# Optimization experiments

Measured on AMD Instinct MI355X. Metric: run time of the kernel, lower is better.

## Reference

```python
import jax, jax.numpy as jnp
import numpy as np
import math

BLOCK = 32
TAU = 0.1
INIT_SPARSITY = 0.1


def setup_inputs() -> dict:
    key = jax.random.key(0)
    k1, k2, k3, k4 = jax.random.split(key, 4)
    B, S, D_IN, D_OUT = 4, 2048, 4096, 4096
    x = jax.random.normal(k1, (B, S, D_IN), dtype=jnp.float32)
    # nn.Linear default init: uniform(-1/sqrt(in), 1/sqrt(in))
    bound = 1.0 / math.sqrt(D_IN)
    weight = jax.random.uniform(k2, (D_OUT, D_IN), minval=-bound, maxval=bound, dtype=jnp.float32)
    bias = jax.random.uniform(k3, (D_OUT,), minval=-bound, maxval=bound, dtype=jnp.float32)
    # scores init per _init_scores: randn*0.1 + logit(init_sparsity)
    target_logit = math.log(INIT_SPARSITY / (1.0 - INIT_SPARSITY))
    scores = jax.random.normal(k4, (D_OUT // BLOCK, D_IN // BLOCK), dtype=jnp.float32) * 0.1 + target_logit
    return {"x": x, "weight": weight, "bias": bias, "scores": scores}


def reference(x, weight, bias, scores):
    # block mask: sigmoid(scores) > tau, expanded 32x32 per block
    block_mask = (jax.nn.sigmoid(scores) > TAU).astype(weight.dtype)  # [O/32, I/32]
    full_mask = jnp.repeat(jnp.repeat(block_mask, BLOCK, axis=0), BLOCK, axis=1)  # [O, I]
    pruned_weight = weight * full_mask
    # F.linear: x @ W^T + b
    return jnp.einsum('bsi,oi->bso', x, pruned_weight) + bias
```

## Files before the change

kernel.cpp:

```cpp
#include <hip/hip_runtime.h>


#define BM 128
#define BN 128
#define BK 64

typedef __attribute__((ext_vector_type(8))) short bf16x8;
typedef __attribute__((ext_vector_type(4))) float f32x4;

__device__ __forceinline__ unsigned short f2bf(float f) {
    union { float f; unsigned u; } v; v.f = f;
    return (unsigned short)((v.u + 0x7FFFu + ((v.u >> 16) & 1u)) >> 16);
}

#define THRESH (-2.1972245773362196f)

__global__ __launch_bounds__(256)
void prep(const float* __restrict__ X, const float* __restrict__ W,
          const float* __restrict__ scores,
          unsigned short* __restrict__ Xb, unsigned short* __restrict__ Wb,
          unsigned long long* __restrict__ mbits,
          int M, int N, int K) {
    const int b   = blockIdx.x;
    const int tid = threadIdx.x;
    const int KBlk = K >> 5;

    if (b < M) {
        const float* src = X + (long)b * K;
        unsigned short* dst = Xb + (long)b * K;
        for (int k = tid * 4; k < K; k += 1024) {
            const float4 a = *(const float4*)(src + k);
            ushort4 p;
            p.x = f2bf(a.x); p.y = f2bf(a.y); p.z = f2bf(a.z); p.w = f2bf(a.w);
            *(ushort4*)(dst + k) = p;
        }
    } else if (b < M + N) {
        const int n = b - M;
        const float* src = W + (long)n * K;
        unsigned short* dst = Wb + (long)n * K;
        const float* srow = scores + (long)(n >> 5) * KBlk;
        for (int k = tid * 4; k < K; k += 1024) {
            if (srow[k >> 5] > THRESH) {
                const float4 a = *(const float4*)(src + k);
                ushort4 p;
                p.x = f2bf(a.x); p.y = f2bf(a.y); p.z = f2bf(a.z); p.w = f2bf(a.w);
                *(ushort4*)(dst + k) = p;
            }
        }
    } else {
        const int nb = (b - (M + N)) * 4 + (tid >> 6);
        const int l  = tid & 63;
        const unsigned long long b0 = __ballot(scores[(long)nb * KBlk + l] > THRESH);
        const unsigned long long b1 = __ballot(scores[(long)nb * KBlk + 64 + l] > THRESH);
        if (l == 0) { mbits[nb * 2] = b0; mbits[nb * 2 + 1] = b1; }
    }
}


__device__ __forceinline__ unsigned long long rfl64(unsigned long long v) {
    unsigned lo = __builtin_amdgcn_readfirstlane((unsigned)v);
    unsigned hi = __builtin_amdgcn_readfirstlane((unsigned)(v >> 32));
    return ((unsigned long long)hi << 32) | lo;
}

#define GLL16(g, l) __builtin_amdgcn_global_load_lds( \
    (const __attribute__((address_space(1))) void*)(g), \
    (__attribute__((address_space(3))) void*)(l), 16, 0, 0)

__global__ __launch_bounds__(256)
void mpl_main(const unsigned short* __restrict__ Xb,
              const unsigned short* __restrict__ Wb,
              const float* __restrict__ bias,
              const unsigned long long* __restrict__ mb,
              float* __restrict__ out, int M, int N, int K)
{
    __shared__ unsigned short sA[BM * BK];
    __shared__ unsigned short sB[BN * BK];

    const int tid  = threadIdx.x;
    const int lane = tid & 63;
    const int wave = tid >> 6;
    const int m0   = blockIdx.y * BM;
    const int n0   = blockIdx.x * BN;
    const int wm   = (wave & 1) * 64;
    const int wn   = (wave >> 1) * 64;
    const long K2  = (long)K * 2;

    const int nbb = n0 >> 5;
    unsigned long long mlo[4], mhi[4];
#pragma unroll
    for (int i = 0; i < 4; i++) {
        mlo[i] = rfl64(mb[(nbb + i) * 2]);
        mhi[i] = rfl64(mb[(nbb + i) * 2 + 1]);
    }

    f32x4 acc[4][4];
#pragma unroll
    for (int i = 0; i < 4; i++)
#pragma unroll
        for (int j = 0; j < 4; j++)
            acc[i][j] = (f32x4){0.f, 0.f, 0.f, 0.f};

    const int r8   = tid >> 3;
    const int cswz = ((tid & 7) ^ ((tid >> 3) & 7)) * 16;
    const char* gA = (const char*)Xb + (long)(m0 + r8) * K2 + cswz;
    const char* gB = (const char*)Wb + (long)(n0 + r8) * K2 + cswz;
    char* sAc = (char*)sA;
    char* sBc = (char*)sB;
    const int ldso = wave * 1024;

    const int fr   = lane & 15;
    const int cxor = lane & 7;
    const int kqc  = lane >> 4;
    const int rowA = wm + fr;
    const int rowB = wn + fr;

    int kb2 = 0;
    for (int half = 0; half < 2; ++half) {
        const unsigned long long w0 = half ? mhi[0] : mlo[0];
        const unsigned long long w1 = half ? mhi[1] : mlo[1];
        const unsigned long long w2 = half ? mhi[2] : mlo[2];
        const unsigned long long w3 = half ? mhi[3] : mlo[3];
        for (int q = 0; q < 32; ++q, ++kb2) {
            const unsigned p0 = (unsigned)(w0 >> (2 * q)) & 3;
            const unsigned p1 = (unsigned)(w1 >> (2 * q)) & 3;
            const unsigned p2 = (unsigned)(w2 >> (2 * q)) & 3;
            const unsigned p3 = (unsigned)(w3 >> (2 * q)) & 3;
            if (!(p0 | p1 | p2 | p3)) continue;

            const long ko = (long)kb2 * 128;
#pragma unroll
            for (int i = 0; i < 4; i++)
                GLL16(gA + (long)i * 32 * K2 + ko, sAc + i * 4096 + ldso);
            if (p0) GLL16(gB + 0L * 32 * K2 + ko, sBc + 0 * 4096 + ldso);
            if (p1) GLL16(gB + 1L * 32 * K2 + ko, sBc + 1 * 4096 + ldso);
            if (p2) GLL16(gB + 2L * 32 * K2 + ko, sBc + 2 * 4096 + ldso);
            if (p3) GLL16(gB + 3L * 32 * K2 + ko, sBc + 3 * 4096 + ldso);
            __syncthreads();

            const unsigned plo = (wave >> 1) ? p2 : p0;
            const unsigned phi = (wave >> 1) ? p3 : p1;

#pragma unroll
            for (int kbl = 0; kbl < 2; ++kbl) {
                if (!(((plo | phi) >> kbl) & 1)) continue;
                const int boff = ((kqc | (kbl << 2)) ^ cxor) * 16;

                bf16x8 af[4];
#pragma unroll
                for (int mi = 0; mi < 4; mi++)
                    af[mi] = *(const bf16x8*)(sAc + (rowA + mi * 16) * 128 + boff);

                if ((plo >> kbl) & 1) {
                    const bf16x8 bf0 = *(const bf16x8*)(sBc + (rowB + 0)  * 128 + boff);
                    const bf16x8 bf1 = *(const bf16x8*)(sBc + (rowB + 16) * 128 + boff);
#pragma unroll
                    for (int mi = 0; mi < 4; mi++) {
                        acc[mi][0] = __builtin_amdgcn_mfma_f32_16x16x32_bf16(af[mi], bf0, acc[mi][0], 0, 0, 0);
                        acc[mi][1] = __builtin_amdgcn_mfma_f32_16x16x32_bf16(af[mi], bf1, acc[mi][1], 0, 0, 0);
                    }
                }
                if ((phi >> kbl) & 1) {
                    const bf16x8 bf2 = *(const bf16x8*)(sBc + (rowB + 32) * 128 + boff);
                    const bf16x8 bf3 = *(const bf16x8*)(sBc + (rowB + 48) * 128 + boff);
#pragma unroll
                    for (int mi = 0; mi < 4; mi++) {
                        acc[mi][2] = __builtin_amdgcn_mfma_f32_16x16x32_bf16(af[mi], bf2, acc[mi][2], 0, 0, 0);
                        acc[mi][3] = __builtin_amdgcn_mfma_f32_16x16x32_bf16(af[mi], bf3, acc[mi][3], 0, 0, 0);
                    }
                }
            }
            __syncthreads();
        }
    }

    const int cn = lane & 15;
    const int rq = (lane >> 4) * 4;
#pragma unroll
    for (int ni = 0; ni < 4; ni++) {
        const int n = n0 + wn + ni * 16 + cn;
        const float b = bias[n];
#pragma unroll
        for (int mi = 0; mi < 4; mi++) {
#pragma unroll
            for (int r = 0; r < 4; r++) {
                const int m = m0 + wm + mi * 16 + rq + r;
                out[(long)m * N + n] = acc[mi][ni][r] + b;
            }
        }
    }
}


#define FBK 32
#define LDSS (FBK + 8)
__global__ __launch_bounds__(256, 2)
void mpl_gemm_fb(const float* __restrict__ X, const float* __restrict__ W,
                 const float* __restrict__ bias, const float* __restrict__ scores,
                 float* __restrict__ out, int M, int N, int K)
{
    __shared__ unsigned short sA[BM * LDSS];
    __shared__ unsigned short sB[BN * LDSS];
    const int tid = threadIdx.x;
    const int m0 = blockIdx.y * BM, n0 = blockIdx.x * BN;
    const int wave = tid >> 6, lane = tid & 63;
    const int wm = (wave & 1) * 64, wn = (wave >> 1) * 64;
    const int kblocks = K >> 5;
    f32x4 acc[4][4];
#pragma unroll
    for (int i = 0; i < 4; i++)
#pragma unroll
        for (int j = 0; j < 4; j++) acc[i][j] = (f32x4){0.f,0.f,0.f,0.f};
    int srow[4], sc4[4], snb[4];
#pragma unroll
    for (int i = 0; i < 4; i++) {
        int f = tid + 256 * i;
        srow[i] = f >> 3; sc4[i] = f & 7; snb[i] = (n0 + srow[i]) >> 5;
    }
    for (int k0 = 0; k0 < K; k0 += FBK) {
        const int kb = k0 >> 5;
#pragma unroll
        for (int i = 0; i < 4; i++) {
            const float4 v = *(const float4*)(X + (long)(m0 + srow[i]) * K + k0 + sc4[i] * 4);
            ushort4 p; p.x = f2bf(v.x); p.y = f2bf(v.y); p.z = f2bf(v.z); p.w = f2bf(v.w);
            *(ushort4*)&sA[srow[i] * LDSS + sc4[i] * 4] = p;
        }
#pragma unroll
        for (int i = 0; i < 4; i++) {
            const float msk = (scores[snb[i] * kblocks + kb] > THRESH) ? 1.0f : 0.0f;
            const float4 v = *(const float4*)(W + (long)(n0 + srow[i]) * K + k0 + sc4[i] * 4);
            ushort4 p; p.x = f2bf(v.x*msk); p.y = f2bf(v.y*msk); p.z = f2bf(v.z*msk); p.w = f2bf(v.w*msk);
            *(ushort4*)&sB[srow[i] * LDSS + sc4[i] * 4] = p;
        }
        __syncthreads();
        const int fr = lane & 15, kq = (lane >> 4) * 8;
        bf16x8 af[4], bfr[4];
#pragma unroll
        for (int mi = 0; mi < 4; mi++) af[mi] = *(const bf16x8*)&sA[(wm + mi*16 + fr) * LDSS + kq];
#pragma unroll
        for (int ni = 0; ni < 4; ni++) bfr[ni] = *(const bf16x8*)&sB[(wn + ni*16 + fr) * LDSS + kq];
#pragma unroll
        for (int mi = 0; mi < 4; mi++)
#pragma unroll
            for (int ni = 0; ni < 4; ni++)
                acc[mi][ni] = __builtin_amdgcn_mfma_f32_16x16x32_bf16(af[mi], bfr[ni], acc[mi][ni], 0,0,0);
        __syncthreads();
    }
    const int cn = lane & 15, rq = (lane >> 4) * 4;
#pragma unroll
    for (int ni = 0; ni < 4; ni++) {
        const int n = n0 + wn + ni * 16 + cn;
        const float b = bias[n];
#pragma unroll
        for (int mi = 0; mi < 4; mi++)
#pragma unroll
            for (int r = 0; r < 4; r++)
                out[(long)(m0 + wm + mi*16 + rq + r) * N + n] = acc[mi][ni][r] + b;
    }
}

extern "C" void kernel_launch(void* const* d_in, const int* in_sizes, int n_in,
                              void* d_out, int out_size, void* d_ws, size_t ws_size,
                              hipStream_t stream) {
    const float* X      = (const float*)d_in[0];
    const float* W      = (const float*)d_in[1];
    const float* bias   = (const float*)d_in[2];
    const float* scores = (const float*)d_in[3];
    float* out          = (float*)d_out;

    const int N = in_sizes[2];
    const int K = in_sizes[1] / N;
    const int M = in_sizes[0] / K;
    const int KB = K >> 5;
    const int NB = N >> 5;

    const size_t mk2 = (size_t)M * K * 2;
    const size_t nk2 = (size_t)N * K * 2;
    const size_t need = mk2 + nk2 + (size_t)NB * 16;

    if (ws_size >= need && KB == 128 && (M % 128) == 0 && (N % 128) == 0 &&
        (K % 1024) == 0 && (NB % 4) == 0) {
        unsigned short* Xb = (unsigned short*)d_ws;
        unsigned short* Wb = (unsigned short*)((char*)d_ws + mk2);
        unsigned long long* mbits = (unsigned long long*)((char*)d_ws + mk2 + nk2);

        prep<<<M + N + NB / 4, 256, 0, stream>>>(X, W, scores, Xb, Wb, mbits, M, N, K);

        dim3 grid(N / BN, M / BM);
        mpl_main<<<grid, dim3(256), 0, stream>>>(Xb, Wb, bias, mbits, out, M, N, K);
    } else {
        dim3 grid(N / BN, M / BM);
        mpl_gemm_fb<<<grid, dim3(256), 0, stream>>>(X, W, bias, scores, out, M, N, K);
    }
}
```

Baseline: 478.1 us.

## Double-buffer LDS tiles with prefetch, remap workgroups across XCDs, stride prep rows

```diff
diff --git a/kernel.cpp b/kernel.cpp
--- a/kernel.cpp
+++ b/kernel.cpp
@@ -25,30 +25,33 @@
     const int tid = threadIdx.x;
     const int KBlk = K >> 5;
 
-    if (b < M) {
-        const float* src = X + (long)b * K;
-        unsigned short* dst = Xb + (long)b * K;
-        for (int k = tid * 4; k < K; k += 1024) {
-            const float4 a = *(const float4*)(src + k);
-            ushort4 p;
-            p.x = f2bf(a.x); p.y = f2bf(a.y); p.z = f2bf(a.z); p.w = f2bf(a.w);
-            *(ushort4*)(dst + k) = p;
-        }
-    } else if (b < M + N) {
-        const int n = b - M;
-        const float* src = W + (long)n * K;
-        unsigned short* dst = Wb + (long)n * K;
-        const float* srow = scores + (long)(n >> 5) * KBlk;
-        for (int k = tid * 4; k < K; k += 1024) {
-            if (srow[k >> 5] > THRESH) {
+    if (b < 2048) {
+        for (int row = b; row < M; row += 2048) {
+            const float* src = X + (long)row * K;
+            unsigned short* dst = Xb + (long)row * K;
+            for (int k = tid * 4; k < K; k += 1024) {
                 const float4 a = *(const float4*)(src + k);
                 ushort4 p;
                 p.x = f2bf(a.x); p.y = f2bf(a.y); p.z = f2bf(a.z); p.w = f2bf(a.w);
                 *(ushort4*)(dst + k) = p;
             }
         }
+    } else if (b < 3072) {
+        for (int row = b - 2048; row < N; row += 1024) {
+            const float* src = W + (long)row * K;
+            unsigned short* dst = Wb + (long)row * K;
+            const float* srow = scores + (long)(row >> 5) * KBlk;
+            for (int k = tid * 4; k < K; k += 1024) {
+                if (srow[k >> 5] > THRESH) {
+                    const float4 a = *(const float4*)(src + k);
+                    ushort4 p;
+                    p.x = f2bf(a.x); p.y = f2bf(a.y); p.z = f2bf(a.z); p.w = f2bf(a.w);
+                    *(ushort4*)(dst + k) = p;
+                }
+            }
+        }
     } else {
-        const int nb = (b - (M + N)) * 4 + (tid >> 6);
+        const int nb = (b - 3072) * 4 + (tid >> 6);
         const int l  = tid & 63;
         const unsigned long long b0 = __ballot(scores[(long)nb * KBlk + l] > THRESH);
         const unsigned long long b1 = __ballot(scores[(long)nb * KBlk + 64 + l] > THRESH);
@@ -66,6 +69,17 @@
 #define GLL16(g, l) __builtin_amdgcn_global_load_lds( \
     (const __attribute__((address_space(1))) void*)(g), \
     (__attribute__((address_space(3))) void*)(l), 16, 0, 0)
+
+#define STAGE(sAbuf, sBbuf, ko) do { \
+    GLL16(gA + 0L * 32 * K2 + (ko), (sAbuf) + 0 * 4096 + ldso); \
+    GLL16(gA + 1L * 32 * K2 + (ko), (sAbuf) + 1 * 4096 + ldso); \
+    GLL16(gA + 2L * 32 * K2 + (ko), (sAbuf) + 2 * 4096 + ldso); \
+    GLL16(gA + 3L * 32 * K2 + (ko), (sAbuf) + 3 * 4096 + ldso); \
+    GLL16(gB + 0L * 32 * K2 + (ko), (sBbuf) + 0 * 4096 + ldso); \
+    GLL16(gB + 1L * 32 * K2 + (ko), (sBbuf) + 1 * 4096 + ldso); \
+    GLL16(gB + 2L * 32 * K2 + (ko), (sBbuf) + 2 * 4096 + ldso); \
+    GLL16(gB + 3L * 32 * K2 + (ko), (sBbuf) + 3 * 4096 + ldso); \
+} while (0)
 
 __global__ __launch_bounds__(256)
 void mpl_main(const unsigned short* __restrict__ Xb,
@@ -74,14 +88,24 @@
               const unsigned long long* __restrict__ mb,
               float* __restrict__ out, int M, int N, int K)
 {
-    __shared__ unsigned short sA[BM * BK];
-    __shared__ unsigned short sB[BN * BK];
+    __shared__ unsigned short sA0[BM * BK];
+    __shared__ unsigned short sB0[BN * BK];
+    __shared__ unsigned short sA1[BM * BK];
+    __shared__ unsigned short sB1[BN * BK];
 
     const int tid  = threadIdx.x;
     const int lane = tid & 63;
     const int wave = tid >> 6;
-    const int m0   = blockIdx.y * BM;
-    const int n0   = blockIdx.x * BN;
+
+    const int nwg = gridDim.x;
+    int L = blockIdx.x;
+    if ((nwg & 7) == 0) L = (L & 7) * (nwg >> 3) + (L >> 3);
+    const int nbx = N / BN;
+    const int bx = L % nbx;
+    const int by = L / nbx;
+
+    const int m0   = by * BM;
+    const int n0   = bx * BN;
     const int wm   = (wave & 1) * 64;
     const int wn   = (wave >> 1) * 64;
     const long K2  = (long)K * 2;
@@ -105,8 +129,10 @@
     const int cswz = ((tid & 7) ^ ((tid >> 3) & 7)) * 16;
     const char* gA = (const char*)Xb + (long)(m0 + r8) * K2 + cswz;
     const char* gB = (const char*)Wb + (long)(n0 + r8) * K2 + cswz;
-    char* sAc = (char*)sA;
-    char* sBc = (char*)sB;
+    char* sA0c = (char*)sA0;
+    char* sB0c = (char*)sB0;
+    char* sA1c = (char*)sA1;
+    char* sB1c = (char*)sB1;
     const int ldso = wave * 1024;
 
     const int fr   = lane & 15;
@@ -115,32 +141,33 @@
     const int rowA = wm + fr;
     const int rowB = wn + fr;
 
-    int kb2 = 0;
-    for (int half = 0; half < 2; ++half) {
-        const unsigned long long w0 = half ? mhi[0] : mlo[0];
-        const unsigned long long w1 = half ? mhi[1] : mlo[1];
-        const unsigned long long w2 = half ? mhi[2] : mlo[2];
-        const unsigned long long w3 = half ? mhi[3] : mlo[3];
-        for (int q = 0; q < 32; ++q, ++kb2) {
-            const unsigned p0 = (unsigned)(w0 >> (2 * q)) & 3;
-            const unsigned p1 = (unsigned)(w1 >> (2 * q)) & 3;
-            const unsigned p2 = (unsigned)(w2 >> (2 * q)) & 3;
-            const unsigned p3 = (unsigned)(w3 >> (2 * q)) & 3;
-            if (!(p0 | p1 | p2 | p3)) continue;
-
-            const long ko = (long)kb2 * 128;
-#pragma unroll
-            for (int i = 0; i < 4; i++)
-                GLL16(gA + (long)i * 32 * K2 + ko, sAc + i * 4096 + ldso);
-            if (p0) GLL16(gB + 0L * 32 * K2 + ko, sBc + 0 * 4096 + ldso);
-            if (p1) GLL16(gB + 1L * 32 * K2 + ko, sBc + 1 * 4096 + ldso);
-            if (p2) GLL16(gB + 2L * 32 * K2 + ko, sBc + 2 * 4096 + ldso);
-            if (p3) GLL16(gB + 3L * 32 * K2 + ko, sBc + 3 * 4096 + ldso);
-            __syncthreads();
-
-            const unsigned plo = (wave >> 1) ? p2 : p0;
-            const unsigned phi = (wave >> 1) ? p3 : p1;
-
+    STAGE(sA0c, sB0c, 0L);
+
+#pragma unroll 2
+    for (int s = 0; s < 64; ++s) {
+        if (s < 63) {
+            const long konext = (long)(s + 1) * 128;
+            if (s & 1) STAGE(sA0c, sB0c, konext);
+            else       STAGE(sA1c, sB1c, konext);
+            asm volatile("s_waitcnt vmcnt(8)" ::: "memory");
+        } else {
+            asm volatile("s_waitcnt vmcnt(0)" ::: "memory");
+        }
+        __builtin_amdgcn_s_barrier();
+        __builtin_amdgcn_sched_barrier(0);
+
+        const char* cA = (s & 1) ? sA1c : sA0c;
+        const char* cB = (s & 1) ? sB1c : sB0c;
+
+        const int hq = s & 31;
+        const unsigned p0 = (unsigned)(((s & 32) ? mhi[0] : mlo[0]) >> (2 * hq)) & 3;
+        const unsigned p1 = (unsigned)(((s & 32) ? mhi[1] : mlo[1]) >> (2 * hq)) & 3;
+        const unsigned p2 = (unsigned)(((s & 32) ? mhi[2] : mlo[2]) >> (2 * hq)) & 3;
+        const unsigned p3 = (unsigned)(((s & 32) ? mhi[3] : mlo[3]) >> (2 * hq)) & 3;
+        const unsigned plo = (wave >> 1) ? p2 : p0;
+        const unsigned phi = (wave >> 1) ? p3 : p1;
+
+        if (plo | phi) {
 #pragma unroll
             for (int kbl = 0; kbl < 2; ++kbl) {
                 if (!(((plo | phi) >> kbl) & 1)) continue;
@@ -149,11 +176,11 @@
                 bf16x8 af[4];
 #pragma unroll
                 for (int mi = 0; mi < 4; mi++)
-                    af[mi] = *(const bf16x8*)(sAc + (rowA + mi * 16) * 128 + boff);
+                    af[mi] = *(const bf16x8*)(cA + (rowA + mi * 16) * 128 + boff);
 
                 if ((plo >> kbl) & 1) {
-                    const bf16x8 bf0 = *(const bf16x8*)(sBc + (rowB + 0)  * 128 + boff);
-                    const bf16x8 bf1 = *(const bf16x8*)(sBc + (rowB + 16) * 128 + boff);
+                    const bf16x8 bf0 = *(const bf16x8*)(cB + (rowB + 0)  * 128 + boff);
+                    const bf16x8 bf1 = *(const bf16x8*)(cB + (rowB + 16) * 128 + boff);
 #pragma unroll
                     for (int mi = 0; mi < 4; mi++) {
                         acc[mi][0] = __builtin_amdgcn_mfma_f32_16x16x32_bf16(af[mi], bf0, acc[mi][0], 0, 0, 0);
@@ -161,8 +188,8 @@
                     }
                 }
                 if ((phi >> kbl) & 1) {
-                    const bf16x8 bf2 = *(const bf16x8*)(sBc + (rowB + 32) * 128 + boff);
-                    const bf16x8 bf3 = *(const bf16x8*)(sBc + (rowB + 48) * 128 + boff);
+                    const bf16x8 bf2 = *(const bf16x8*)(cB + (rowB + 32) * 128 + boff);
+                    const bf16x8 bf3 = *(const bf16x8*)(cB + (rowB + 48) * 128 + boff);
 #pragma unroll
                     for (int mi = 0; mi < 4; mi++) {
                         acc[mi][2] = __builtin_amdgcn_mfma_f32_16x16x32_bf16(af[mi], bf2, acc[mi][2], 0, 0, 0);
@@ -170,8 +197,9 @@
                     }
                 }
             }
-            __syncthreads();
-        }
+        }
+        __builtin_amdgcn_sched_barrier(0);
+        __builtin_amdgcn_s_barrier();
     }
 
     const int cn = lane & 15;
@@ -284,10 +312,9 @@
         unsigned short* Wb = (unsigned short*)((char*)d_ws + mk2);
         unsigned long long* mbits = (unsigned long long*)((char*)d_ws + mk2 + nk2);
 
-        prep<<<M + N + NB / 4, 256, 0, stream>>>(X, W, scores, Xb, Wb, mbits, M, N, K);
-
-        dim3 grid(N / BN, M / BM);
-        mpl_main<<<grid, dim3(256), 0, stream>>>(Xb, Wb, bias, mbits, out, M, N, K);
+        prep<<<3072 + NB / 4, 256, 0, stream>>>(X, W, scores, Xb, Wb, mbits, M, N, K);
+
+        mpl_main<<<dim3((N / BN) * (M / BM)), dim3(256), 0, stream>>>(Xb, Wb, bias, mbits, out, M, N, K);
     } else {
         dim3 grid(N / BN, M / BM);
         mpl_gemm_fb<<<grid, dim3(256), 0, stream>>>(X, W, bias, scores, out, M, N, K);
```

Result: slower. 569.3 us (+19.1%).

## Fuse fp32-to-bf16 conversion into GEMM tile loads, drop prep pass

Applied to the files above, without the earlier changes.

```diff
diff --git a/kernel.cpp b/kernel.cpp
--- a/kernel.cpp
+++ b/kernel.cpp
@@ -13,47 +13,22 @@
     return (unsigned short)((v.u + 0x7FFFu + ((v.u >> 16) & 1u)) >> 16);
 }
 
+__device__ __forceinline__ unsigned cvtpk(float lo, float hi) {
+    unsigned r;
+    asm("v_cvt_pk_bf16_f32 %0, %1, %2" : "=v"(r) : "v"(lo), "v"(hi));
+    return r;
+}
+
 #define THRESH (-2.1972245773362196f)
 
 __global__ __launch_bounds__(256)
-void prep(const float* __restrict__ X, const float* __restrict__ W,
-          const float* __restrict__ scores,
-          unsigned short* __restrict__ Xb, unsigned short* __restrict__ Wb,
-          unsigned long long* __restrict__ mbits,
-          int M, int N, int K) {
-    const int b   = blockIdx.x;
-    const int tid = threadIdx.x;
-    const int KBlk = K >> 5;
-
-    if (b < M) {
-        const float* src = X + (long)b * K;
-        unsigned short* dst = Xb + (long)b * K;
-        for (int k = tid * 4; k < K; k += 1024) {
-            const float4 a = *(const float4*)(src + k);
-            ushort4 p;
-            p.x = f2bf(a.x); p.y = f2bf(a.y); p.z = f2bf(a.z); p.w = f2bf(a.w);
-            *(ushort4*)(dst + k) = p;
-        }
-    } else if (b < M + N) {
-        const int n = b - M;
-        const float* src = W + (long)n * K;
-        unsigned short* dst = Wb + (long)n * K;
-        const float* srow = scores + (long)(n >> 5) * KBlk;
-        for (int k = tid * 4; k < K; k += 1024) {
-            if (srow[k >> 5] > THRESH) {
-                const float4 a = *(const float4*)(src + k);
-                ushort4 p;
-                p.x = f2bf(a.x); p.y = f2bf(a.y); p.z = f2bf(a.z); p.w = f2bf(a.w);
-                *(ushort4*)(dst + k) = p;
-            }
-        }
-    } else {
-        const int nb = (b - (M + N)) * 4 + (tid >> 6);
-        const int l  = tid & 63;
-        const unsigned long long b0 = __ballot(scores[(long)nb * KBlk + l] > THRESH);
-        const unsigned long long b1 = __ballot(scores[(long)nb * KBlk + 64 + l] > THRESH);
-        if (l == 0) { mbits[nb * 2] = b0; mbits[nb * 2 + 1] = b1; }
-    }
+void packmask(const float* __restrict__ scores, unsigned long long* __restrict__ mbits,
+              int KBlk) {
+    const int nb = blockIdx.x * 4 + (threadIdx.x >> 6);
+    const int l  = threadIdx.x & 63;
+    const unsigned long long b0 = __ballot(scores[(long)nb * KBlk + l] > THRESH);
+    const unsigned long long b1 = __ballot(scores[(long)nb * KBlk + 64 + l] > THRESH);
+    if (l == 0) { mbits[nb * 2] = b0; mbits[nb * 2 + 1] = b1; }
 }
 
 
@@ -63,16 +38,14 @@
     return ((unsigned long long)hi << 32) | lo;
 }
 
-#define GLL16(g, l) __builtin_amdgcn_global_load_lds( \
-    (const __attribute__((address_space(1))) void*)(g), \
-    (__attribute__((address_space(3))) void*)(l), 16, 0, 0)
+#define PB(i, s) ((unsigned)((((s) & 32) ? mhi[i] : mlo[i]) >> (2 * ((s) & 31))) & 3)
 
 __global__ __launch_bounds__(256)
-void mpl_main(const unsigned short* __restrict__ Xb,
-              const unsigned short* __restrict__ Wb,
-              const float* __restrict__ bias,
-              const unsigned long long* __restrict__ mb,
-              float* __restrict__ out, int M, int N, int K)
+void mpl_fused(const float* __restrict__ X,
+               const float* __restrict__ W,
+               const float* __restrict__ bias,
+               const unsigned long long* __restrict__ mb,
+               float* __restrict__ out, int M, int N, int K)
 {
     __shared__ unsigned short sA[BM * BK];
     __shared__ unsigned short sB[BN * BK];
@@ -84,7 +57,6 @@
     const int n0   = blockIdx.x * BN;
     const int wm   = (wave & 1) * 64;
     const int wn   = (wave >> 1) * 64;
-    const long K2  = (long)K * 2;
 
     const int nbb = n0 >> 5;
     unsigned long long mlo[4], mhi[4];
@@ -101,13 +73,15 @@
         for (int j = 0; j < 4; j++)
             acc[i][j] = (f32x4){0.f, 0.f, 0.f, 0.f};
 
-    const int r8   = tid >> 3;
-    const int cswz = ((tid & 7) ^ ((tid >> 3) & 7)) * 16;
-    const char* gA = (const char*)Xb + (long)(m0 + r8) * K2 + cswz;
-    const char* gB = (const char*)Wb + (long)(n0 + r8) * K2 + cswz;
+    const int rl  = tid >> 4;
+    const int g   = tid & 15;
+    const float* pa = X + (long)(m0 + rl) * K + g * 4;
+    const float* pb = W + (long)(n0 + rl) * K + g * 4;
+    const int swz = ((((g >> 1) ^ (rl & 7)) << 4) | ((g & 1) << 3));
+    char* lA = (char*)sA + rl * 128 + swz;
+    char* lB = (char*)sB + rl * 128 + swz;
     char* sAc = (char*)sA;
     char* sBc = (char*)sB;
-    const int ldso = wave * 1024;
 
     const int fr   = lane & 15;
     const int cxor = lane & 7;
@@ -115,32 +89,33 @@
     const int rowA = wm + fr;
     const int rowB = wn + fr;
 
-    int kb2 = 0;
-    for (int half = 0; half < 2; ++half) {
-        const unsigned long long w0 = half ? mhi[0] : mlo[0];
-        const unsigned long long w1 = half ? mhi[1] : mlo[1];
-        const unsigned long long w2 = half ? mhi[2] : mlo[2];
-        const unsigned long long w3 = half ? mhi[3] : mlo[3];
-        for (int q = 0; q < 32; ++q, ++kb2) {
-            const unsigned p0 = (unsigned)(w0 >> (2 * q)) & 3;
-            const unsigned p1 = (unsigned)(w1 >> (2 * q)) & 3;
-            const unsigned p2 = (unsigned)(w2 >> (2 * q)) & 3;
-            const unsigned p3 = (unsigned)(w3 >> (2 * q)) & 3;
-            if (!(p0 | p1 | p2 | p3)) continue;
-
-            const long ko = (long)kb2 * 128;
-#pragma unroll
-            for (int i = 0; i < 4; i++)
-                GLL16(gA + (long)i * 32 * K2 + ko, sAc + i * 4096 + ldso);
-            if (p0) GLL16(gB + 0L * 32 * K2 + ko, sBc + 0 * 4096 + ldso);
-            if (p1) GLL16(gB + 1L * 32 * K2 + ko, sBc + 1 * 4096 + ldso);
-            if (p2) GLL16(gB + 2L * 32 * K2 + ko, sBc + 2 * 4096 + ldso);
-            if (p3) GLL16(gB + 3L * 32 * K2 + ko, sBc + 3 * 4096 + ldso);
-            __syncthreads();
-
-            const unsigned plo = (wave >> 1) ? p2 : p0;
-            const unsigned phi = (wave >> 1) ? p3 : p1;
-
+    for (int s = 0; s < 64; ++s) {
+        const unsigned c0 = PB(0, s), c1 = PB(1, s), c2 = PB(2, s), c3 = PB(3, s);
+        if (!(c0 | c1 | c2 | c3)) continue;
+
+        const int ks = s * 64;
+#pragma unroll
+        for (int i = 0; i < 8; i++) {
+            const float4 v = *(const float4*)(pa + (long)i * 16 * K + ks);
+            uint2 u; u.x = cvtpk(v.x, v.y); u.y = cvtpk(v.z, v.w);
+            *(uint2*)(lA + i * 2048) = u;
+        }
+#pragma unroll
+        for (int j = 0; j < 8; j++) {
+            const unsigned pj = (j >> 1) == 0 ? c0 : (j >> 1) == 1 ? c1
+                              : (j >> 1) == 2 ? c2 : c3;
+            if (pj) {
+                const float4 v = *(const float4*)(pb + (long)j * 16 * K + ks);
+                uint2 u; u.x = cvtpk(v.x, v.y); u.y = cvtpk(v.z, v.w);
+                *(uint2*)(lB + j * 2048) = u;
+            }
+        }
+        __syncthreads();
+
+        const unsigned plo = (wave >> 1) ? c2 : c0;
+        const unsigned phi = (wave >> 1) ? c3 : c1;
+
+        if (plo | phi) {
 #pragma unroll
             for (int kbl = 0; kbl < 2; ++kbl) {
                 if (!(((plo | phi) >> kbl) & 1)) continue;
@@ -170,8 +145,8 @@
                     }
                 }
             }
-            __syncthreads();
-        }
+        }
+        __syncthreads();
     }
 
     const int cn = lane & 15;
@@ -274,20 +249,16 @@
     const int KB = K >> 5;
     const int NB = N >> 5;
 
-    const size_t mk2 = (size_t)M * K * 2;
-    const size_t nk2 = (size_t)N * K * 2;
-    const size_t need = mk2 + nk2 + (size_t)NB * 16;
+    const size_t need = (size_t)NB * 16;
 
     if (ws_size >= need && KB == 128 && (M % 128) == 0 && (N % 128) == 0 &&
-        (K % 1024) == 0 && (NB % 4) == 0) {
-        unsigned short* Xb = (unsigned short*)d_ws;
-        unsigned short* Wb = (unsigned short*)((char*)d_ws + mk2);
-        unsigned long long* mbits = (unsigned long long*)((char*)d_ws + mk2 + nk2);
-
-        prep<<<M + N + NB / 4, 256, 0, stream>>>(X, W, scores, Xb, Wb, mbits, M, N, K);
+        (NB % 4) == 0) {
+        unsigned long long* mbits = (unsigned long long*)d_ws;
+
+        packmask<<<NB / 4, 256, 0, stream>>>(scores, mbits, KB);
 
         dim3 grid(N / BN, M / BM);
-        mpl_main<<<grid, dim3(256), 0, stream>>>(Xb, Wb, bias, mbits, out, M, N, K);
+        mpl_fused<<<grid, dim3(256), 0, stream>>>(X, W, bias, mbits, out, M, N, K);
     } else {
         dim3 grid(N / BN, M / BM);
         mpl_gemm_fb<<<grid, dim3(256), 0, stream>>>(X, W, bias, scores, out, M, N, K);
```

After: 678.5 us. 41.9% more time.
